# Performance work log

Hardware: AMD Instinct MI355X
Metric: run time of the kernel (lower is better)

## Reference

```python
import jax, jax.numpy as jnp
import numpy as np


def topk_activation(x, k):
    # x: [B, L]; keep top-k per row, zeros elsewhere (torch.topk + scatter_)
    vals, idx = jax.lax.top_k(x, k)            # [B, k]
    rows = jnp.arange(x.shape[0])[:, None]     # [B, 1]
    return jnp.zeros_like(x).at[rows, idx].set(vals)


def setup_inputs() -> dict:
    key = jax.random.key(0)
    k0, k1, k2, k3 = jax.random.split(key, 4)
    B, n_in, n_lat = 4096, 768, 24576
    x = jax.random.normal(k0, (B, n_in), dtype=jnp.float32)
    b = jnp.zeros((n_in,), jnp.float32)
    W_enc = jax.random.normal(k1, (n_lat, n_in), dtype=jnp.float32) * 0.02
    b_enc = jnp.zeros((n_lat,), jnp.float32)
    W_dec = jax.random.normal(k2, (n_in, n_lat), dtype=jnp.float32) * 0.02
    # unit L2 norm per decoder column (as in _normalize_decoder)
    W_dec = W_dec / jnp.clip(jnp.linalg.norm(W_dec, axis=0, keepdims=True), 1e-8)
    miss_counts = jax.random.randint(k3, (n_lat,), 0, 2)  # ~half 'dead' (>=1)
    return {"x": x, "b": b, "W_enc": W_enc, "b_enc": b_enc, "W_dec": W_dec,
            "miss_counts": miss_counts, "k": 32, "aux_k": 512}


def reference(x, b, W_enc, b_enc, W_dec, miss_counts, k, aux_k):
    x_centered = x - b                                   # [B, n_in]
    alpha_pre = x_centered @ W_enc.T + b_enc             # [B, n_lat]
    alpha = topk_activation(alpha_pre, k)                # sparse code
    x_hat = alpha @ W_dec.T + b                          # dense decode
    fired_mask = alpha != 0
    # aux dead-feature path; dead_mask = miss_counts >= threshold(=1).
    # With the chosen miss_counts fill, dead count >> aux_k, so
    # min(aux_k, dead.sum()) == aux_k (static for jit).
    dead_mask = miss_counts >= 1                         # [n_lat]
    alpha_pre_dead = jnp.where(dead_mask[None, :], alpha_pre, -jnp.inf)
    alpha_aux = topk_activation(alpha_pre_dead, aux_k)
    aux_x_hat = alpha_aux @ W_dec.T + b
    return x_hat, alpha, fired_mask, aux_x_hat
```

## Files before the change

kernel.cpp:

```cpp
#include <hip/hip_runtime.h>
#include <math.h>

#define NB   4096
#define NIN  768
#define NLAT 24576
#define K2   768
#define KT2  12

#define BM 128
#define BN 128
#define BK 16
#define LDT 132

#define CAND_CAP 512
#define BAND_CAP 160
#define MAIN_CAP 64
#define AUX_CAP  1024
#define SELT     1024
#define GRP      6

#define CM_CAP 768
#define CA_CAP 1536
#define BB_CAP 256
#define BPSTRIDE (BAND_CAP + 4)

#define OFF_K16  0
#define OFF_REDF 49152
#define OFF_CTRL 49664
#define OFF_PCNT 49792
#define OFF_CKM  50176
#define OFF_CIM  52224
#define OFF_CKA  54272
#define OFF_CIA  56320
#define OFF_BIM  58368
#define OFF_BIA  59008
#define OFF_BVM  59648
#define OFF_BVA  60928
#define OFF_BSM  62208
#define OFF_BSA  62368
#define OFF_REDI 62528
#define SMEM_SEL 62592

typedef __bf16 bf16x8 __attribute__((ext_vector_type(8)));
typedef float  f32x4  __attribute__((ext_vector_type(4)));

__device__ __forceinline__ unsigned fkey(float f) {
  unsigned u = __float_as_uint(f);
  return u ^ ((unsigned)((int)u >> 31) | 0x80000000u);
}
__device__ __forceinline__ float keyinv(unsigned u) {
  unsigned s = (u & 0x80000000u) ? (u ^ 0x80000000u) : ~u;
  return __uint_as_float(s);
}
__device__ __forceinline__ float zup(float p) {
  p = fminf(fmaxf(p, 1e-7f), 0.5f);
  float t = sqrtf(-2.0f * logf(p));
  return t - (2.30753f + 0.27061f * t) / (1.0f + 0.99229f * t + 0.04481f * t * t);
}

#define GLOAD16(g, l) __builtin_amdgcn_global_load_lds( \
    (const __attribute__((address_space(1))) unsigned int*)(g), \
    (__attribute__((address_space(3))) unsigned int*)(l), 16, 0, 0)

__global__ __launch_bounds__(256) void k_deadbits(const int* __restrict__ miss,
                                                  unsigned* __restrict__ bits) {
  int j = blockIdx.x * 256 + threadIdx.x;
  unsigned long long b = __ballot(miss[j] >= 1);
  if ((threadIdx.x & 63) == 0) {
    int w = j >> 5;
    bits[w] = (unsigned)b;
    bits[w + 1] = (unsigned)(b >> 32);
  }
}

__global__ __launch_bounds__(256) void k_ndead(const unsigned* __restrict__ bits,
                                               int* __restrict__ out) {
  __shared__ int w[4];
  int t = threadIdx.x;
  int c = 0;
  for (int i = t; i < NLAT / 32; i += 256) c += __popc(bits[i]);
#pragma unroll
  for (int o = 32; o; o >>= 1) c += __shfl_xor(c, o);
  if ((t & 63) == 0) w[t >> 6] = c;
  __syncthreads();
  if (t == 0) out[0] = w[0] + w[1] + w[2] + w[3];
}

__global__ __launch_bounds__(256) void k_transpose(const float* __restrict__ src,
                                                   __bf16* __restrict__ dst) {
  __shared__ float tile[32][33];
  int bx = blockIdx.x * 32;
  int by = blockIdx.y * 32;
  int tx = threadIdx.x, ty = threadIdx.y;
  for (int i = ty; i < 32; i += 8)
    tile[i][tx] = src[(size_t)(by + i) * NLAT + bx + tx];
  __syncthreads();
  for (int i = ty; i < 32; i += 8)
    dst[(size_t)(bx + i) * NIN + by + tx] = (__bf16)tile[tx][i];
}

__global__ __launch_bounds__(256) void k_pack_a(const float* __restrict__ x,
    const float* __restrict__ bvec, __bf16* __restrict__ A2) {
  const int mt = blockIdx.x, kt = blockIdx.y, t = threadIdx.x;
  __bf16* out = A2 + (((size_t)mt * KT2 + kt) << 13);
#pragma unroll
  for (int i = 0; i < 32; ++i) {
    int idx = i * 256 + t;
    int r = idx >> 6, c2 = idx & 63;
    int kk = c2 ^ ((r & 7) << 3);
    int k = kt * 64 + kk;
    float v = x[(size_t)(mt * 128 + r) * NIN + k] - bvec[k];
    out[idx] = (__bf16)v;
  }
}

__global__ __launch_bounds__(256) void k_pack_b(const float* __restrict__ We,
    __bf16* __restrict__ B2) {
  const int nt = blockIdx.x, kt = blockIdx.y, t = threadIdx.x;
  __bf16* out = B2 + (((size_t)nt * KT2 + kt) << 13);
#pragma unroll
  for (int i = 0; i < 32; ++i) {
    int idx = i * 256 + t;
    int r = idx >> 6, c2 = idx & 63;
    int kk = c2 ^ ((r & 7) << 3);
    int k = kt * 64 + kk;
    float v = We[(size_t)(nt * 128 + r) * NIN + k];
    out[idx] = (__bf16)v;
  }
}

__global__ __launch_bounds__(256) void k_gemm_bf16(
    const __bf16* __restrict__ A2, const __bf16* __restrict__ B2,
    const float* __restrict__ be, float* __restrict__ apre) {
  __shared__ char sA[16384];
  __shared__ char sB[16384];
  const int t = threadIdx.x;
  const int lane = t & 63, wave = t >> 6;
  int flat = blockIdx.y * 32 + blockIdx.x;
  int nf = (flat & 7) * 768 + (flat >> 3);
  const int mt = nf & 31, nt = nf >> 5;
  const int wm = wave >> 1, wn = wave & 1;

  int aoff[4][2], boff[4][2];
#pragma unroll
  for (int f = 0; f < 4; ++f) {
    int ra = wm * 64 + f * 16 + (lane & 15);
    int rb = wn * 64 + f * 16 + (lane & 15);
#pragma unroll
    for (int kk = 0; kk < 2; ++kk) {
      int c = kk * 64 + (lane >> 4) * 16;
      aoff[f][kk] = ra * 128 + (c ^ ((ra & 7) << 4));
      boff[f][kk] = rb * 128 + (c ^ ((rb & 7) << 4));
    }
  }
  f32x4 acc[4][4] = {};
  const char* gA = (const char*)(A2 + (((size_t)mt * KT2) << 13));
  const char* gB = (const char*)(B2 + (((size_t)nt * KT2) << 13));
  for (int kt = 0; kt < KT2; ++kt) {
    const char* tA = gA + ((size_t)kt << 14);
    const char* tB = gB + ((size_t)kt << 14);
#pragma unroll
    for (int i = 0; i < 4; ++i) {
      int chunk = (i * 4 + wave) * 1024;
      GLOAD16(tA + chunk + lane * 16, sA + chunk);
      GLOAD16(tB + chunk + lane * 16, sB + chunk);
    }
    __syncthreads();
#pragma unroll
    for (int kk = 0; kk < 2; ++kk) {
      bf16x8 a[4], b[4];
#pragma unroll
      for (int f = 0; f < 4; ++f) {
        a[f] = *(const bf16x8*)(sA + aoff[f][kk]);
        b[f] = *(const bf16x8*)(sB + boff[f][kk]);
      }
#pragma unroll
      for (int mi = 0; mi < 4; ++mi)
#pragma unroll
        for (int ni = 0; ni < 4; ++ni)
          acc[mi][ni] = __builtin_amdgcn_mfma_f32_16x16x32_bf16(a[mi], b[ni], acc[mi][ni], 0, 0, 0);
    }
    __syncthreads();
  }
  const int m0 = mt * 128 + wm * 64, n0 = nt * 128 + wn * 64;
#pragma unroll
  for (int ni = 0; ni < 4; ++ni) {
    int n = n0 + ni * 16 + (lane & 15);
    float bb = be[n];
#pragma unroll
    for (int mi = 0; mi < 4; ++mi) {
      int mbase = m0 + mi * 16 + (lane >> 4) * 4;
#pragma unroll
      for (int q = 0; q < 4; ++q)
        apre[(size_t)(mbase + q) * NLAT + n] = acc[mi][ni][q] + bb;
    }
  }
}

__global__ __launch_bounds__(256) void k_encgemm_f32(
    const float* __restrict__ x, const float* __restrict__ bvec,
    const float* __restrict__ We, const float* __restrict__ be,
    float* __restrict__ apre) {
  __shared__ float As[BK][LDT];
  __shared__ float Bs[BK][LDT];
  const int t = threadIdx.x;
  const int m0 = blockIdx.x * BM;
  const int n0 = blockIdx.y * BN;
  const int lane = t & 63, wave = t >> 6;
  const int cn = ((wave & 1) * 8 + (lane & 7)) * 8;
  const int cm = ((wave >> 1) * 8 + (lane >> 3)) * 8;
  float acc[8][8] = {};
  const float* xb = x + (size_t)m0 * NIN;
  const float* wb = We + (size_t)n0 * NIN;
  for (int k0 = 0; k0 < NIN; k0 += BK) {
#pragma unroll
    for (int i = 0; i < 2; ++i) {
      int e = t + i * 256;
      int row = e >> 2, q = e & 3;
      float4 bv = *(const float4*)(bvec + k0 + q * 4);
      float4 av = *(const float4*)(xb + (size_t)row * NIN + k0 + q * 4);
      av.x -= bv.x; av.y -= bv.y; av.z -= bv.z; av.w -= bv.w;
      As[q * 4 + 0][row] = av.x; As[q * 4 + 1][row] = av.y;
      As[q * 4 + 2][row] = av.z; As[q * 4 + 3][row] = av.w;
      float4 wv = *(const float4*)(wb + (size_t)row * NIN + k0 + q * 4);
      Bs[q * 4 + 0][row] = wv.x; Bs[q * 4 + 1][row] = wv.y;
      Bs[q * 4 + 2][row] = wv.z; Bs[q * 4 + 3][row] = wv.w;
    }
    __syncthreads();
#pragma unroll
    for (int kk = 0; kk < BK; ++kk) {
      float a0[8], b0[8];
      *(float4*)&a0[0] = *(const float4*)&As[kk][cm];
      *(float4*)&a0[4] = *(const float4*)&As[kk][cm + 4];
      *(float4*)&b0[0] = *(const float4*)&Bs[kk][cn];
      *(float4*)&b0[4] = *(const float4*)&Bs[kk][cn + 4];
#pragma unroll
      for (int i = 0; i < 8; ++i)
#pragma unroll
        for (int j = 0; j < 8; ++j)
          acc[i][j] = fmaf(a0[i], b0[j], acc[i][j]);
    }
    __syncthreads();
  }
  float bb[8];
  *(float4*)&bb[0] = *(const float4*)(be + n0 + cn);
  *(float4*)&bb[4] = *(const float4*)(be + n0 + cn + 4);
#pragma unroll
  for (int i = 0; i < 8; ++i) {
    float4 v0 = make_float4(acc[i][0] + bb[0], acc[i][1] + bb[1],
                            acc[i][2] + bb[2], acc[i][3] + bb[3]);
    float4 v1 = make_float4(acc[i][4] + bb[4], acc[i][5] + bb[5],
                            acc[i][6] + bb[6], acc[i][7] + bb[7]);
    float* orow = apre + (size_t)(m0 + cm + i) * NLAT + n0 + cn;
    *(float4*)orow = v0;
    *(float4*)(orow + 4) = v1;
  }
}

__global__ __launch_bounds__(1024) void k_select16(
    const float* __restrict__ apre, const float* __restrict__ x,
    const float* __restrict__ bvec, const float* __restrict__ We,
    const float* __restrict__ be, const unsigned* __restrict__ dbits,
    const int* __restrict__ kptr, const int* __restrict__ akptr,
    const int* __restrict__ ndeadP,
    int* __restrict__ cnts, int* __restrict__ mIdxG, float* __restrict__ mValG,
    int* __restrict__ aIdxG, float* __restrict__ aValG,
    int* __restrict__ bandP, int* __restrict__ flags) {
  __shared__ float redF[32];
  __shared__ float statF[4];
  __shared__ int ctrl[24];
  __shared__ int histM[256];
  __shared__ int histA[256];
  __shared__ uint2 cM[CM_CAP];
  __shared__ uint2 cA[CA_CAP];
  __shared__ uint2 bbM[BB_CAP];
  __shared__ uint2 bbA[BB_CAP];
  __shared__ int biM[BAND_CAP];
  __shared__ int biA[BAND_CAP];
  __shared__ double bvM[BAND_CAP];
  __shared__ double bvA[BAND_CAP];
  __shared__ unsigned char bsM[BAND_CAP];
  __shared__ unsigned char bsA[BAND_CAP];
  unsigned* uctrl = (unsigned*)ctrl;

  const int t = threadIdx.x;
  const int r = blockIdx.x;
  const int lane = t & 63, wave = t >> 6;

  if (t < 24) ctrl[t] = 0;
  if (t >= 256 && t < 512) histM[t - 256] = 0;
  else if (t >= 512 && t < 768) histA[t - 512] = 0;

  const uint4* rowp = (const uint4*)(apre + (size_t)r * NLAT);
  unsigned dm = 0;
  float s1 = 0.f, s2 = 0.f;
#pragma unroll
  for (int i = 0; i < GRP; ++i) {
    int g = t + SELT * i;
    uint4 rv = rowp[g];
    unsigned nb = (dbits[g >> 3] >> ((g & 7) * 4)) & 0xFu;
    dm |= nb << (4 * i);
    float vs[4] = {__uint_as_float(rv.x), __uint_as_float(rv.y),
                   __uint_as_float(rv.z), __uint_as_float(rv.w)};
#pragma unroll
    for (int q = 0; q < 4; ++q) { float v = vs[q]; s1 += v; s2 += v * v; }
  }
#pragma unroll
  for (int o = 32; o; o >>= 1) { s1 += __shfl_xor(s1, o); s2 += __shfl_xor(s2, o); }
  if (lane == 0) { redF[wave] = s1; redF[16 + wave] = s2; }
  __syncthreads();
  if (wave == 0) {
    float a0 = (lane < 16) ? redF[lane] : 0.f;
    float a1 = (lane < 16) ? redF[16 + lane] : 0.f;
#pragma unroll
    for (int o = 32; o; o >>= 1) { a0 += __shfl_xor(a0, o); a1 += __shfl_xor(a1, o); }
    if (lane == 0) {
      float mu = a0 / (float)NLAT;
      float var = fmaxf(a1 / (float)NLAT - mu * mu, 1e-20f);
      statF[0] = mu; statF[1] = sqrtf(var);
    }
  }
  __syncthreads();

  int kmain = kptr[0]; if (kmain > MAIN_CAP) kmain = MAIN_CAP;
  int kaux  = akptr[0]; if (kaux > AUX_CAP)  kaux  = AUX_CAP;
  const int ndead = ndeadP[0];
  int kauxE = kaux > ndead ? ndead : kaux;
  const bool mainOn = (kmain > 0);
  const bool auxOn  = (kauxE > 0);
  const float mu = statF[0], sg = statF[1];
  unsigned TkM = 0xFFFFFFFFu, TkA = 0xFFFFFFFFu;
  if (mainOn) TkM = fkey(mu + sg * zup(8.f * kmain / (float)NLAT));
  if (auxOn) {
    float facA = (3.f * kauxE > 1280.f) ? 2.f : 3.f;
    TkA = fkey(mu + sg * zup(facA * kauxE / (float)ndead));
  }

  unsigned mxM = 0u, mxA = 0u;
#pragma unroll
  for (int i = 0; i < GRP; ++i) {
    int g = t + SELT * i;
    uint4 rv = rowp[g];
    unsigned nb = (dm >> (4 * i)) & 0xFu;
    float vs[4] = {__uint_as_float(rv.x), __uint_as_float(rv.y),
                   __uint_as_float(rv.z), __uint_as_float(rv.w)};
#pragma unroll
    for (int q = 0; q < 4; ++q) {
      unsigned kk = fkey(vs[q]);
      unsigned j = (unsigned)(4 * g + q);
      if (mainOn && kk >= TkM) {
        mxM = kk > mxM ? kk : mxM;
        int p = atomicAdd(&ctrl[0], 1);
        if (p < CM_CAP) { cM[p].x = kk; cM[p].y = j; }
      }
      if (auxOn && ((nb >> q) & 1u) && kk >= TkA) {
        mxA = kk > mxA ? kk : mxA;
        int p = atomicAdd(&ctrl[1], 1);
        if (p < CA_CAP) { cA[p].x = kk; cA[p].y = j; }
      }
    }
  }
#pragma unroll
  for (int o = 32; o; o >>= 1) {
    unsigned a = __shfl_xor(mxM, o); mxM = a > mxM ? a : mxM;
    unsigned b = __shfl_xor(mxA, o); mxA = b > mxA ? b : mxA;
  }
  if (lane == 0) { atomicMax(&uctrl[10], mxM); atomicMax(&uctrl[11], mxA); }
  __syncthreads();
  int ccM = ctrl[0], ccA = ctrl[1];
  bool ok = (!mainOn || (ccM >= kmain && ccM <= CM_CAP)) &&
            (!auxOn  || (ccA >= kauxE && ccA <= CA_CAP));
  if (!ok) { if (t == 0) flags[r] = 1; return; }
  if (!auxOn) ccA = 0;
  if (!mainOn) ccM = 0;
  unsigned MxM = uctrl[10], MxA = uctrl[11];
  float sclM = 255.0f / fmaxf((float)(MxM - TkM) + 1.0f, 1.0f);
  float sclA = 255.0f / fmaxf((float)(MxA - TkA) + 1.0f, 1.0f);

  for (int c = t; c < ccM; c += 1024) {
    int b = (int)((float)(cM[c].x - TkM) * sclM);
    b = b < 0 ? 0 : (b > 255 ? 255 : b);
    atomicAdd(&histM[b], 1);
  }
  for (int c = t; c < ccA; c += 1024) {
    int b = (int)((float)(cA[c].x - TkA) * sclA);
    b = b < 0 ? 0 : (b > 255 ? 255 : b);
    atomicAdd(&histA[b], 1);
  }
  __syncthreads();
  if (t == 0 && mainOn) {
    int above = 0, b = 0;
    for (int i = 255; i >= 0; --i) {
      if (above + histM[i] >= kmain) { b = i; break; }
      above += histM[i];
    }
    ctrl[12] = b; ctrl[13] = above;
  }
  if (t == 64 && auxOn) {
    int above = 0, b = 0;
    for (int i = 255; i >= 0; --i) {
      if (above + histA[i] >= kauxE) { b = i; break; }
      above += histA[i];
    }
    ctrl[14] = b; ctrl[15] = above;
  }
  __syncthreads();
  int bM = ctrl[12], aboveM = ctrl[13];
  int bA = ctrl[14], aboveA = ctrl[15];
  for (int c = t; c < ccM; c += 1024) {
    int b = (int)((float)(cM[c].x - TkM) * sclM);
    b = b < 0 ? 0 : (b > 255 ? 255 : b);
    if (b == bM) {
      int p = atomicAdd(&ctrl[16], 1);
      if (p < BB_CAP) bbM[p] = cM[c];
    }
  }
  for (int c = t; c < ccA; c += 1024) {
    int b = (int)((float)(cA[c].x - TkA) * sclA);
    b = b < 0 ? 0 : (b > 255 ? 255 : b);
    if (b == bA) {
      int p = atomicAdd(&ctrl[17], 1);
      if (p < BB_CAP) bbA[p] = cA[c];
    }
  }
  __syncthreads();
  int nbM = ctrl[16], nbA = ctrl[17];
  if ((mainOn && nbM > BB_CAP) || (auxOn && nbA > BB_CAP)) {
    if (t == 0) flags[r] = 1;
    return;
  }
  if (!mainOn) nbM = 0;
  if (!auxOn) nbA = 0;
  if (t < nbM) {
    uint2 e = bbM[t];
    int rank = 0;
    for (int qq = 0; qq < nbM; ++qq) {
      uint2 f = bbM[qq];
      rank += (f.x > e.x || (f.x == e.x && (int)f.y < (int)e.y)) ? 1 : 0;
    }
    if (rank == kmain - aboveM - 1) ctrl[2] = (int)e.x;
  }
  if (t >= 512 && t - 512 < nbA) {
    uint2 e = bbA[t - 512];
    int rank = 0;
    for (int qq = 0; qq < nbA; ++qq) {
      uint2 f = bbA[qq];
      rank += (f.x > e.x || (f.x == e.x && (int)f.y < (int)e.y)) ? 1 : 0;
    }
    if (rank == kauxE - aboveA - 1) ctrl[3] = (int)e.x;
  }
  __syncthreads();

  float VsM = keyinv((unsigned)ctrl[2]);
  float epsM = 1.5e-2f + 2e-3f * fabsf(VsM);
  unsigned KhiBM = mainOn ? fkey(VsM + epsM) : 0xFFFFFFFFu;
  unsigned KloBM = mainOn ? fkey(VsM - epsM) : 0xFFFFFFFFu;
  float VsA = keyinv((unsigned)ctrl[3]);
  float epsA = 1.5e-2f + 2e-3f * fabsf(VsA);
  unsigned KhiBA = auxOn ? fkey(VsA + epsA) : 0xFFFFFFFFu;
  unsigned KloBA = auxOn ? fkey(VsA - epsA) : 0xFFFFFFFFu;
  for (int c = t; c < ccM; c += 1024) {
    unsigned kk = cM[c].x;
    if (kk > KhiBM) atomicAdd(&ctrl[4], 1);
    else if (kk >= KloBM) {
      int p = atomicAdd(&ctrl[5], 1);
      if (p < BAND_CAP) biM[p] = (int)cM[c].y;
    }
  }
  for (int c = t; c < ccA; c += 1024) {
    unsigned kk = cA[c].x;
    if (kk > KhiBA) atomicAdd(&ctrl[6], 1);
    else if (kk >= KloBA) {
      int p = atomicAdd(&ctrl[7], 1);
      if (p < BAND_CAP) biA[p] = (int)cA[c].y;
    }
  }
  __syncthreads();
  if ((mainOn && ctrl[5] > BAND_CAP) || (auxOn && ctrl[7] > BAND_CAP)) {
    if (t == 0) flags[r] = 1;
    return;
  }
  if (t == 0) flags[r] = 0;
  int nAbM = ctrl[4], bcM = ctrl[5];
  int nAbA = ctrl[6], bcA = ctrl[7];
  if (!mainOn) bcM = 0;
  if (!auxOn) bcA = 0;
  int needBM = kmain - nAbM; if (needBM < 0) needBM = 0; if (needBM > bcM) needBM = bcM;
  int needBA = kauxE - nAbA; if (needBA < 0) needBA = 0; if (needBA > bcA) needBA = bcA;

  {
    const float* xr = x + (size_t)r * NIN;
    float xb[NIN / 64];
#pragma unroll
    for (int jj = 0; jj < NIN / 64; ++jj) {
      int col = lane + 64 * jj;
      xb[jj] = xr[col] - bvec[col];
    }
    int tot = bcM + bcA;
    for (int m = wave; m < tot; m += 16) {
      int j = (m < bcM) ? biM[m] : biA[m - bcM];
      const float* wr = We + (size_t)j * NIN;
      double s = 0.0;
#pragma unroll
      for (int jj = 0; jj < NIN / 64; ++jj)
        s += (double)xb[jj] * (double)wr[lane + 64 * jj];
#pragma unroll
      for (int o = 32; o; o >>= 1) s += __shfl_xor(s, o);
      if (lane == 0) {
        if (m < bcM) bvM[m] = s + (double)be[j];
        else bvA[m - bcM] = s + (double)be[j];
      }
    }
  }
  __syncthreads();
  if (t < bcM) {
    double vi = bvM[t]; int ii = biM[t];
    double tie = fabs(vi) * 4e-8 + 1e-12;
    int rank = 0;
    for (int qq = 0; qq < bcM; ++qq) {
      double d = bvM[qq] - vi;
      rank += ((fabs(d) <= tie) ? (biM[qq] < ii) : (d > 0.0)) ? 1 : 0;
    }
    bsM[t] = (rank < needBM) ? 1 : 0;
  }
  if (t >= 512 && t - 512 < bcA) {
    int tt = t - 512;
    double vi = bvA[tt]; int ii = biA[tt];
    double tie = fabs(vi) * 4e-8 + 1e-12;
    int rank = 0;
    for (int qq = 0; qq < bcA; ++qq) {
      double d = bvA[qq] - vi;
      rank += ((fabs(d) <= tie) ? (biA[qq] < ii) : (d > 0.0)) ? 1 : 0;
    }
    bsA[tt] = (rank < needBA) ? 1 : 0;
  }
  __syncthreads();

  for (int c = t; c < ccM; c += 1024) {
    unsigned kk = cM[c].x; int j = (int)cM[c].y;
    bool sel = kk > KhiBM;
    if (!sel && kk >= KloBM) {
      for (int m2 = 0; m2 < bcM; ++m2)
        if (biM[m2] == j) { sel = bsM[m2] != 0; break; }
    }
    float v = keyinv(kk);
    if (sel && v != 0.0f) {
      int p = atomicAdd(&ctrl[8], 1);
      if (p < MAIN_CAP) { mIdxG[r * MAIN_CAP + p] = j; mValG[r * MAIN_CAP + p] = v; }
    }
  }
  for (int c = t; c < ccA; c += 1024) {
    unsigned kk = cA[c].x; int j = (int)cA[c].y;
    bool sel = kk > KhiBA;
    if (!sel && kk >= KloBA) {
      for (int m2 = 0; m2 < bcA; ++m2)
        if (biA[m2] == j) { sel = bsA[m2] != 0; break; }
    }
    float v = keyinv(kk);
    if (sel && v != 0.0f) {
      int p = atomicAdd(&ctrl[9], 1);
      if (p < AUX_CAP) { aIdxG[r * AUX_CAP + p] = j; aValG[r * AUX_CAP + p] = v; }
    }
  }
  __syncthreads();
  int* bp = bandP + (size_t)r * BPSTRIDE;
  if (t == 0) {
    cnts[2 * r] = ctrl[8] < MAIN_CAP ? ctrl[8] : MAIN_CAP;
    cnts[2 * r + 1] = auxOn ? (ctrl[9] < AUX_CAP ? ctrl[9] : AUX_CAP) : 0;
    bp[0] = (int)KhiBM; bp[1] = (int)KloBM; bp[2] = bcM;
  }
  if (t < bcM) bp[3 + t] = (biM[t] << 1) | (int)bsM[t];
}

__global__ __launch_bounds__(256) void k_emit(
    const float* apre, const int* __restrict__ flags,
    const int* __restrict__ bandP, float* __restrict__ alpha, float* mask) {
  const int bid = blockIdx.x;
  const int r = bid / 3, c = bid % 3;
  if (flags[r]) return;
  __shared__ int hdr[3];
  __shared__ int bent[BAND_CAP];
  const int t = threadIdx.x;
  const int* bp = bandP + (size_t)r * BPSTRIDE;
  if (t < 3) hdr[t] = bp[t];
  __syncthreads();
  int bc = hdr[2];
  if (t < bc) bent[t] = bp[3 + t];
  __syncthreads();
  unsigned KhiB = (unsigned)hdr[0], KloB = (unsigned)hdr[1];
  const float4* src = (const float4*)(apre + (size_t)r * NLAT) + c * 2048;
  float4* adst = (float4*)(alpha + (size_t)r * NLAT) + c * 2048;
  float4* mdst = (float4*)(mask + (size_t)r * NLAT) + c * 2048;
  const int ebase = c * 8192;
#pragma unroll
  for (int i = 0; i < 8; ++i) {
    int g = t + 256 * i;
    float4 v4 = src[g];
    float vs[4] = {v4.x, v4.y, v4.z, v4.w};
    float av[4], mv[4];
#pragma unroll
    for (int q = 0; q < 4; ++q) {
      float v = vs[q];
      unsigned kk = fkey(v);
      int j = ebase + 4 * g + q;
      bool sel = kk > KhiB;
      if (!sel && kk >= KloB) {
        for (int m = 0; m < bc; ++m)
          if ((bent[m] >> 1) == j) { sel = (bent[m] & 1) != 0; break; }
      }
      av[q] = sel ? v : 0.0f;
      mv[q] = (sel && v != 0.0f) ? 1.0f : 0.0f;
    }
    adst[g] = make_float4(av[0], av[1], av[2], av[3]);
    mdst[g] = make_float4(mv[0], mv[1], mv[2], mv[3]);
  }
}

__global__ __launch_bounds__(SELT) void k_selectFB(
    const float* apre, const float* __restrict__ x,
    const float* __restrict__ bvec, const float* __restrict__ We,
    const float* __restrict__ be, const unsigned* __restrict__ dbits,
    const int* __restrict__ kptr, const int* __restrict__ akptr,
    float* __restrict__ alpha, float* mask,
    int* __restrict__ cnts, int* __restrict__ mIdxG, float* __restrict__ mValG,
    int* __restrict__ aIdxG, float* __restrict__ aValG,
    const int* __restrict__ flags) {
  if (flags[blockIdx.x] == 0) return;
  extern __shared__ char smem[];
  uint2*    keys2 = (uint2*)(smem + OFF_K16);
  float*    redF  = (float*)(smem + OFF_REDF);
  int*      redI  = (int*)(smem + OFF_REDI);
  int*      ctrl  = (int*)(smem + OFF_CTRL);
  float*    ctrlF = (float*)(smem + OFF_CTRL);
  int*      pcnt  = (int*)(smem + OFF_PCNT);
  unsigned* ckM   = (unsigned*)(smem + OFF_CKM);
  int*      ciM   = (int*)(smem + OFF_CIM);
  unsigned* ckA   = (unsigned*)(smem + OFF_CKA);
  int*      ciA   = (int*)(smem + OFF_CIA);
  int*      biM   = (int*)(smem + OFF_BIM);
  int*      biA   = (int*)(smem + OFF_BIA);
  double*   bvM   = (double*)(smem + OFF_BVM);
  double*   bvA   = (double*)(smem + OFF_BVA);
  unsigned char* bsM = (unsigned char*)(smem + OFF_BSM);
  unsigned char* bsA = (unsigned char*)(smem + OFF_BSA);

  const int t = threadIdx.x;
  const int r = blockIdx.x;
  const int lane = t & 63, wave = t >> 6;

  if (t < 96) pcnt[t] = 0;
  else if (t < 108) ctrl[t - 96] = 0;

  const uint4* rowp = (const uint4*)(apre + (size_t)r * NLAT);
  const float* rowf = apre + (size_t)r * NLAT;
  unsigned dm = 0;
  float s1 = 0.f, s2 = 0.f;
  float vmxA = -INFINITY, vmnA = INFINITY, vmxD = -INFINITY, vmnD = INFINITY;
#pragma unroll
  for (int i = 0; i < GRP; ++i) {
    int g = t + SELT * i;
    uint4 rv = rowp[g];
    unsigned nb = (dbits[g >> 3] >> ((g & 7) * 4)) & 0xFu;
    dm |= nb << (4 * i);
    float vs[4] = {__uint_as_float(rv.x), __uint_as_float(rv.y),
                   __uint_as_float(rv.z), __uint_as_float(rv.w)};
    unsigned k16[4];
#pragma unroll
    for (int q = 0; q < 4; ++q) {
      float v = vs[q];
      k16[q] = fkey(v) >> 16;
      s1 += v; s2 += v * v;
      vmxA = fmaxf(vmxA, v); vmnA = fminf(vmnA, v);
      if ((nb >> q) & 1u) { vmxD = fmaxf(vmxD, v); vmnD = fminf(vmnD, v); }
    }
    uint2 kp2;
    kp2.x = k16[0] | (k16[1] << 16);
    kp2.y = k16[2] | (k16[3] << 16);
    keys2[g] = kp2;
  }
  int nd = __popc(dm & 0xFFFFFFu);
#pragma unroll
  for (int o = 32; o; o >>= 1) {
    s1 += __shfl_xor(s1, o); s2 += __shfl_xor(s2, o);
    vmxA = fmaxf(vmxA, __shfl_xor(vmxA, o)); vmnA = fminf(vmnA, __shfl_xor(vmnA, o));
    vmxD = fmaxf(vmxD, __shfl_xor(vmxD, o)); vmnD = fminf(vmnD, __shfl_xor(vmnD, o));
    nd += __shfl_xor(nd, o);
  }
  if (lane == 0) {
    float* rf = redF + wave * 8;
    rf[0] = s1; rf[1] = s2; rf[2] = vmxA; rf[3] = vmnA; rf[4] = vmxD; rf[5] = vmnD;
    redI[wave] = nd;
  }
  __syncthreads();
  if (wave == 0) {
    float a0 = 0.f, a1 = 0.f, a2 = -INFINITY, a3 = INFINITY, a4 = -INFINITY, a5 = INFINITY;
    int a6 = 0;
    if (lane < 16) {
      const float* rf = redF + lane * 8;
      a0 = rf[0]; a1 = rf[1]; a2 = rf[2]; a3 = rf[3]; a4 = rf[4]; a5 = rf[5];
      a6 = redI[lane];
    }
#pragma unroll
    for (int o = 32; o; o >>= 1) {
      a0 += __shfl_xor(a0, o); a1 += __shfl_xor(a1, o);
      a2 = fmaxf(a2, __shfl_xor(a2, o)); a3 = fminf(a3, __shfl_xor(a3, o));
      a4 = fmaxf(a4, __shfl_xor(a4, o)); a5 = fminf(a5, __shfl_xor(a5, o));
      a6 += __shfl_xor(a6, o);
    }
    if (lane == 0) {
      float mu = a0 / (float)NLAT;
      float var = fmaxf(a1 / (float)NLAT - mu * mu, 1e-20f);
      ctrlF[16] = mu; ctrlF[17] = sqrtf(var);
      ctrlF[18] = a3; ctrlF[19] = a2;
      ctrlF[20] = a5; ctrlF[21] = a4;
      ctrl[22] = a6;
    }
  }
  __syncthreads();

  int kmain = kptr[0]; if (kmain > MAIN_CAP) kmain = MAIN_CAP;
  int kaux  = akptr[0]; if (kaux > AUX_CAP)  kaux  = AUX_CAP;
  const float mu = ctrlF[16], sg = ctrlF[17];
  const int ndead = ctrl[22];
  int kauxE = kaux > ndead ? ndead : kaux;
  const bool mainOn = (kmain > 0);
  const bool auxOn  = (kauxE > 0);

  unsigned TloM = fkey(ctrlF[18]) >> 16, ThiM = (fkey(ctrlF[19]) >> 16) + 1u;
  int cLoM = NLAT, cHiM = 0;
  unsigned TloA = 0u, ThiA = 2u;
  int cLoA = 0, cHiA = 0;
  if (auxOn) { TloA = fkey(ctrlF[20]) >> 16; ThiA = (fkey(ctrlF[21]) >> 16) + 1u; cLoA = ndead; }

  for (int it = 0; it < 16; ++it) {
    bool actM = mainOn && (cLoM - cHiM) > (CAND_CAP - 8) && (ThiM - TloM) > 1u;
    bool actA = auxOn  && (cLoA - cHiA) > (CAND_CAP - 8) && (ThiA - TloA) > 1u;
    if (!actM && !actA) break;
    unsigned TM1 = TloM + 1u, TM2 = TM1, TM3 = TM1;
    unsigned TA1 = TloA + 1u, TA2 = TA1, TA3 = TA1;
    if (actM) {
      unsigned lo1 = TloM + 1u, hi1 = ThiM - 1u;
      if (it == 0) {
        float fn = (float)NLAT;
        TM1 = fkey(mu + sg * zup(4.f * kmain / fn)) >> 16;
        TM2 = fkey(mu + sg * zup((float)kmain / fn)) >> 16;
        TM3 = fkey(mu + sg * zup(0.25f * kmain / fn)) >> 16;
      } else {
        float vlo = keyinv(TloM << 16), vhi = keyinv((ThiM << 16) - 1u);
        TM1 = fkey(0.75f * vlo + 0.25f * vhi) >> 16;
        TM2 = fkey(0.50f * vlo + 0.50f * vhi) >> 16;
        TM3 = fkey(0.25f * vlo + 0.75f * vhi) >> 16;
      }
      TM1 = TM1 < lo1 ? lo1 : (TM1 > hi1 ? hi1 : TM1);
      TM2 = TM2 < TM1 ? TM1 : (TM2 > hi1 ? hi1 : TM2);
      TM3 = TM3 < TM2 ? TM2 : (TM3 > hi1 ? hi1 : TM3);
    }
    if (actA) {
      unsigned lo1 = TloA + 1u, hi1 = ThiA - 1u;
      if (it == 0) {
        float fn = (float)ndead;
        TA1 = fkey(mu + sg * zup(4.f * kauxE / fn)) >> 16;
        TA2 = fkey(mu + sg * zup((float)kauxE / fn)) >> 16;
        TA3 = fkey(mu + sg * zup(0.25f * kauxE / fn)) >> 16;
      } else {
        float vlo = keyinv(TloA << 16), vhi = keyinv((ThiA << 16) - 1u);
        TA1 = fkey(0.75f * vlo + 0.25f * vhi) >> 16;
        TA2 = fkey(0.50f * vlo + 0.50f * vhi) >> 16;
        TA3 = fkey(0.25f * vlo + 0.75f * vhi) >> 16;
      }
      TA1 = TA1 < lo1 ? lo1 : (TA1 > hi1 ? hi1 : TA1);
      TA2 = TA2 < TA1 ? TA1 : (TA2 > hi1 ? hi1 : TA2);
      TA3 = TA3 < TA2 ? TA2 : (TA3 > hi1 ? hi1 : TA3);
    }
    int cm1 = 0, cm2 = 0, cm3 = 0, ca1 = 0, ca2 = 0, ca3 = 0;
#pragma unroll
    for (int i = 0; i < GRP; ++i) {
      uint2 kv = keys2[t + SELT * i];
      unsigned nb = (dm >> (4 * i)) & 0xFu;
      unsigned ks[4] = {kv.x & 0xFFFFu, kv.x >> 16, kv.y & 0xFFFFu, kv.y >> 16};
#pragma unroll
      for (int q = 0; q < 4; ++q) {
        unsigned kk = ks[q];
        cm1 += (kk >= TM1); cm2 += (kk >= TM2); cm3 += (kk >= TM3);
        if ((nb >> q) & 1u) { ca1 += (kk >= TA1); ca2 += (kk >= TA2); ca3 += (kk >= TA3); }
      }
    }
#pragma unroll
    for (int o = 32; o; o >>= 1) {
      cm1 += __shfl_xor(cm1, o); cm2 += __shfl_xor(cm2, o); cm3 += __shfl_xor(cm3, o);
      ca1 += __shfl_xor(ca1, o); ca2 += __shfl_xor(ca2, o); ca3 += __shfl_xor(ca3, o);
    }
    if (lane == 0) {
      int* pc = pcnt + it * 6;
      atomicAdd(&pc[0], cm1); atomicAdd(&pc[1], cm2); atomicAdd(&pc[2], cm3);
      atomicAdd(&pc[3], ca1); atomicAdd(&pc[4], ca2); atomicAdd(&pc[5], ca3);
    }
    __syncthreads();
    const int* pc = pcnt + it * 6;
    int CM1 = pc[0], CM2 = pc[1], CM3 = pc[2];
    int CA1 = pc[3], CA2 = pc[4], CA3 = pc[5];
    if (actM) {
      if (CM3 >= kmain)      { TloM = TM3; cLoM = CM3; }
      else if (CM2 >= kmain) { TloM = TM2; cLoM = CM2; ThiM = TM3; cHiM = CM3; }
      else if (CM1 >= kmain) { TloM = TM1; cLoM = CM1; ThiM = TM2; cHiM = CM2; }
      else                   { ThiM = TM1; cHiM = CM1; }
    }
    if (actA) {
      if (CA3 >= kauxE)      { TloA = TA3; cLoA = CA3; }
      else if (CA2 >= kauxE) { TloA = TA2; cLoA = CA2; ThiA = TA3; cHiA = CA3; }
      else if (CA1 >= kauxE) { TloA = TA1; cLoA = CA1; ThiA = TA2; cHiA = CA2; }
      else                   { ThiA = TA1; cHiA = CA1; }
    }
  }

#pragma unroll
  for (int i = 0; i < GRP; ++i) {
    int g = t + SELT * i;
    uint2 kv = keys2[g];
    unsigned nb = (dm >> (4 * i)) & 0xFu;
    unsigned ks[4] = {kv.x & 0xFFFFu, kv.x >> 16, kv.y & 0xFFFFu, kv.y >> 16};
#pragma unroll
    for (int q = 0; q < 4; ++q) {
      unsigned kk = ks[q];
      int j = 4 * g + q;
      if (mainOn && kk >= TloM && kk < ThiM) {
        int p = atomicAdd(&ctrl[0], 1);
        if (p < CAND_CAP) { ckM[p] = fkey(rowf[j]); ciM[p] = j; }
      }
      if (auxOn && ((nb >> q) & 1u) && kk >= TloA && kk < ThiA) {
        int p = atomicAdd(&ctrl[1], 1);
        if (p < CAND_CAP) { ckA[p] = fkey(rowf[j]); ciA[p] = j; }
      }
    }
  }
  __syncthreads();
  int ccM = ctrl[0] < CAND_CAP ? ctrl[0] : CAND_CAP;
  int ccA = ctrl[1] < CAND_CAP ? ctrl[1] : CAND_CAP;
  int needM = kmain - cHiM; if (needM < 1) needM = 1; if (needM > ccM) needM = ccM;
  int needA = kauxE - cHiA; if (needA < 1) needA = 1; if (needA > ccA) needA = ccA;

  if (t < ccM) {
    unsigned ki = ckM[t]; int ii = ciM[t];
    int rank = 0;
    for (int qq = 0; qq < ccM; ++qq) {
      unsigned kq = ckM[qq];
      rank += (kq > ki || (kq == ki && ciM[qq] < ii)) ? 1 : 0;
    }
    if (rank == needM - 1) ctrl[2] = (int)ki;
  } else if (t >= 512 && t - 512 < ccA) {
    int tt = t - 512;
    unsigned ki = ckA[tt]; int ii = ciA[tt];
    int rank = 0;
    for (int qq = 0; qq < ccA; ++qq) {
      unsigned kq = ckA[qq];
      rank += (kq > ki || (kq == ki && ciA[qq] < ii)) ? 1 : 0;
    }
    if (rank == needA - 1) ctrl[3] = (int)ki;
  }
  __syncthreads();

  float VsM = keyinv((unsigned)ctrl[2]);
  float epsM = 1.5e-2f + 2e-3f * fabsf(VsM);
  unsigned KhiBM = mainOn ? fkey(VsM + epsM) : 0xFFFFFFFFu;
  unsigned KloBM = mainOn ? fkey(VsM - epsM) : 0xFFFFFFFFu;
  float VsA = keyinv((unsigned)ctrl[3]);
  float epsA = 1.5e-2f + 2e-3f * fabsf(VsA);
  unsigned KhiBA = auxOn ? fkey(VsA + epsA) : 0xFFFFFFFFu;
  unsigned KloBA = auxOn ? fkey(VsA - epsA) : 0xFFFFFFFFu;
  unsigned KhiBM16 = KhiBM >> 16, KloBM16 = KloBM >> 16;
  unsigned KhiBA16 = KhiBA >> 16, KloBA16 = KloBA >> 16;
  int abvM = 0, abvA = 0;
#pragma unroll
  for (int i = 0; i < GRP; ++i) {
    int g = t + SELT * i;
    uint2 kv = keys2[g];
    unsigned nb = (dm >> (4 * i)) & 0xFu;
    unsigned ks[4] = {kv.x & 0xFFFFu, kv.x >> 16, kv.y & 0xFFFFu, kv.y >> 16};
#pragma unroll
    for (int q = 0; q < 4; ++q) {
      unsigned kk = ks[q];
      int j = 4 * g + q;
      if (mainOn) {
        if (kk > KhiBM16) ++abvM;
        else if (kk >= KloBM16) {
          unsigned kf = fkey(rowf[j]);
          if (kf > KhiBM) ++abvM;
          else if (kf >= KloBM) {
            int p = atomicAdd(&ctrl[5], 1);
            if (p < BAND_CAP) biM[p] = j;
          }
        }
      }
      if (auxOn && ((nb >> q) & 1u)) {
        if (kk > KhiBA16) ++abvA;
        else if (kk >= KloBA16) {
          unsigned kf = fkey(rowf[j]);
          if (kf > KhiBA) ++abvA;
          else if (kf >= KloBA) {
            int p = atomicAdd(&ctrl[7], 1);
            if (p < BAND_CAP) biA[p] = j;
          }
        }
      }
    }
  }
#pragma unroll
  for (int o = 32; o; o >>= 1) { abvM += __shfl_xor(abvM, o); abvA += __shfl_xor(abvA, o); }
  if (lane == 0) { atomicAdd(&ctrl[4], abvM); atomicAdd(&ctrl[6], abvA); }
  __syncthreads();
  int nAbM = ctrl[4], bcM = ctrl[5] < BAND_CAP ? ctrl[5] : BAND_CAP;
  int nAbA = ctrl[6], bcA = auxOn ? (ctrl[7] < BAND_CAP ? ctrl[7] : BAND_CAP) : 0;
  if (!mainOn) bcM = 0;
  int needBM = kmain - nAbM; if (needBM < 0) needBM = 0; if (needBM > bcM) needBM = bcM;
  int needBA = kauxE - nAbA; if (needBA < 0) needBA = 0; if (needBA > bcA) needBA = bcA;

  {
    const float* xr = x + (size_t)r * NIN;
    float xb[NIN / 64];
#pragma unroll
    for (int jj = 0; jj < NIN / 64; ++jj) {
      int col = lane + 64 * jj;
      xb[jj] = xr[col] - bvec[col];
    }
    int tot = bcM + bcA;
    for (int m = wave; m < tot; m += 16) {
      int j = (m < bcM) ? biM[m] : biA[m - bcM];
      const float* wr = We + (size_t)j * NIN;
      double s = 0.0;
#pragma unroll
      for (int jj = 0; jj < NIN / 64; ++jj)
        s += (double)xb[jj] * (double)wr[lane + 64 * jj];
#pragma unroll
      for (int o = 32; o; o >>= 1) s += __shfl_xor(s, o);
      if (lane == 0) {
        if (m < bcM) bvM[m] = s + (double)be[j];
        else bvA[m - bcM] = s + (double)be[j];
      }
    }
  }
  __syncthreads();
  if (t < bcM) {
    double vi = bvM[t]; int ii = biM[t];
    double tie = fabs(vi) * 4e-8 + 1e-12;
    int rank = 0;
    for (int qq = 0; qq < bcM; ++qq) {
      double d = bvM[qq] - vi;
      rank += ((fabs(d) <= tie) ? (biM[qq] < ii) : (d > 0.0)) ? 1 : 0;
    }
    bsM[t] = (rank < needBM) ? 1 : 0;
  } else if (t >= 512 && t - 512 < bcA) {
    int tt = t - 512;
    double vi = bvA[tt]; int ii = biA[tt];
    double tie = fabs(vi) * 4e-8 + 1e-12;
    int rank = 0;
    for (int qq = 0; qq < bcA; ++qq) {
      double d = bvA[qq] - vi;
      rank += ((fabs(d) <= tie) ? (biA[qq] < ii) : (d > 0.0)) ? 1 : 0;
    }
    bsA[tt] = (rank < needBA) ? 1 : 0;
  }
  __syncthreads();

  {
    float4* arow = (float4*)(alpha + (size_t)r * NLAT);
    float4* mrow = (float4*)(mask + (size_t)r * NLAT);
#pragma unroll
    for (int i = 0; i < GRP; ++i) {
      int g = t + SELT * i;
      uint4 rv = rowp[g];
      unsigned nb = (dm >> (4 * i)) & 0xFu;
      float vs[4] = {__uint_as_float(rv.x), __uint_as_float(rv.y),
                     __uint_as_float(rv.z), __uint_as_float(rv.w)};
      float av[4], mv[4];
#pragma unroll
      for (int q = 0; q < 4; ++q) {
        float v = vs[q];
        unsigned kk = fkey(v);
        int j = 4 * g + q;
        bool selM = mainOn && (kk > KhiBM);
        if (mainOn && !selM && kk >= KloBM) {
          for (int m2 = 0; m2 < bcM; ++m2)
            if (biM[m2] == j) { selM = bsM[m2] != 0; break; }
        }
        bool nz = selM && (v != 0.0f);
        av[q] = selM ? v : 0.0f;
        mv[q] = nz ? 1.0f : 0.0f;
        if (nz) {
          int p = atomicAdd(&ctrl[8], 1);
          if (p < MAIN_CAP) { mIdxG[r * MAIN_CAP + p] = j; mValG[r * MAIN_CAP + p] = v; }
        }
        if (auxOn && ((nb >> q) & 1u)) {
          bool selA = kk > KhiBA;
          if (!selA && kk >= KloBA) {
            for (int m2 = 0; m2 < bcA; ++m2)
              if (biA[m2] == j) { selA = bsA[m2] != 0; break; }
          }
          if (selA && v != 0.0f) {
            int p = atomicAdd(&ctrl[9], 1);
            if (p < AUX_CAP) { aIdxG[r * AUX_CAP + p] = j; aValG[r * AUX_CAP + p] = v; }
          }
        }
      }
      arow[g] = make_float4(av[0], av[1], av[2], av[3]);
      mrow[g] = make_float4(mv[0], mv[1], mv[2], mv[3]);
    }
  }
  __syncthreads();
  if (t == 0) {
    cnts[2 * r] = ctrl[8] < MAIN_CAP ? ctrl[8] : MAIN_CAP;
    cnts[2 * r + 1] = auxOn ? (ctrl[9] < AUX_CAP ? ctrl[9] : AUX_CAP) : 0;
  }
}

__global__ __launch_bounds__(256) void k_decode(
    const int* __restrict__ cnts, const int* __restrict__ mIdxG,
    const float* __restrict__ mValG, const int* __restrict__ aIdxG,
    const float* __restrict__ aValG, const float* __restrict__ bvec,
    const __bf16* __restrict__ Wt, const float* __restrict__ Wd,
    float* __restrict__ xhat, float* __restrict__ auxo) {
  const int r = blockIdx.x, t = threadIdx.x;
  __shared__ int sMi[MAIN_CAP];
  __shared__ float sMv[MAIN_CAP];
  __shared__ int sAi[AUX_CAP];
  __shared__ float sAv[AUX_CAP];
  int kc = cnts[2 * r], ac = cnts[2 * r + 1];
  if (t < MAIN_CAP && t < kc) { sMi[t] = mIdxG[r * MAIN_CAP + t]; sMv[t] = mValG[r * MAIN_CAP + t]; }
  for (int i = t; i < ac; i += 256) { sAi[i] = aIdxG[r * AUX_CAP + i]; sAv[i] = aValG[r * AUX_CAP + i]; }
  __syncthreads();

  float o0 = 0.f, o1 = 0.f, o2 = 0.f;
  float a0 = 0.f, a1 = 0.f, a2 = 0.f;
  if (Wt) {
    int i = 0;
    for (; i + 4 <= kc; i += 4) {
      int i0 = sMi[i], i1 = sMi[i + 1], i2 = sMi[i + 2], i3 = sMi[i + 3];
      float v0 = sMv[i], v1 = sMv[i + 1], v2 = sMv[i + 2], v3 = sMv[i + 3];
      const __bf16* p0 = Wt + (size_t)i0 * NIN;
      const __bf16* p1 = Wt + (size_t)i1 * NIN;
      const __bf16* p2 = Wt + (size_t)i2 * NIN;
      const __bf16* p3 = Wt + (size_t)i3 * NIN;
      float w00 = p0[t], w01 = p0[t + 256], w02 = p0[t + 512];
      float w10 = p1[t], w11 = p1[t + 256], w12 = p1[t + 512];
      float w20 = p2[t], w21 = p2[t + 256], w22 = p2[t + 512];
      float w30 = p3[t], w31 = p3[t + 256], w32 = p3[t + 512];
      o0 = fmaf(v0, w00, o0); o1 = fmaf(v0, w01, o1); o2 = fmaf(v0, w02, o2);
      o0 = fmaf(v1, w10, o0); o1 = fmaf(v1, w11, o1); o2 = fmaf(v1, w12, o2);
      o0 = fmaf(v2, w20, o0); o1 = fmaf(v2, w21, o1); o2 = fmaf(v2, w22, o2);
      o0 = fmaf(v3, w30, o0); o1 = fmaf(v3, w31, o1); o2 = fmaf(v3, w32, o2);
    }
    for (; i < kc; ++i) {
      const __bf16* p = Wt + (size_t)sMi[i] * NIN;
      float v = sMv[i];
      o0 = fmaf(v, (float)p[t], o0);
      o1 = fmaf(v, (float)p[t + 256], o1);
      o2 = fmaf(v, (float)p[t + 512], o2);
    }
    i = 0;
    for (; i + 4 <= ac; i += 4) {
      int i0 = sAi[i], i1 = sAi[i + 1], i2 = sAi[i + 2], i3 = sAi[i + 3];
      float v0 = sAv[i], v1 = sAv[i + 1], v2 = sAv[i + 2], v3 = sAv[i + 3];
      const __bf16* p0 = Wt + (size_t)i0 * NIN;
      const __bf16* p1 = Wt + (size_t)i1 * NIN;
      const __bf16* p2 = Wt + (size_t)i2 * NIN;
      const __bf16* p3 = Wt + (size_t)i3 * NIN;
      float w00 = p0[t], w01 = p0[t + 256], w02 = p0[t + 512];
      float w10 = p1[t], w11 = p1[t + 256], w12 = p1[t + 512];
      float w20 = p2[t], w21 = p2[t + 256], w22 = p2[t + 512];
      float w30 = p3[t], w31 = p3[t + 256], w32 = p3[t + 512];
      a0 = fmaf(v0, w00, a0); a1 = fmaf(v0, w01, a1); a2 = fmaf(v0, w02, a2);
      a0 = fmaf(v1, w10, a0); a1 = fmaf(v1, w11, a1); a2 = fmaf(v1, w12, a2);
      a0 = fmaf(v2, w20, a0); a1 = fmaf(v2, w21, a1); a2 = fmaf(v2, w22, a2);
      a0 = fmaf(v3, w30, a0); a1 = fmaf(v3, w31, a1); a2 = fmaf(v3, w32, a2);
    }
    for (; i < ac; ++i) {
      const __bf16* p = Wt + (size_t)sAi[i] * NIN;
      float v = sAv[i];
      a0 = fmaf(v, (float)p[t], a0);
      a1 = fmaf(v, (float)p[t + 256], a1);
      a2 = fmaf(v, (float)p[t + 512], a2);
    }
  } else {
    for (int i = 0; i < kc; ++i) {
      float v = sMv[i]; int ix = sMi[i];
      o0 = fmaf(v, Wd[(size_t)t * NLAT + ix], o0);
      o1 = fmaf(v, Wd[(size_t)(t + 256) * NLAT + ix], o1);
      o2 = fmaf(v, Wd[(size_t)(t + 512) * NLAT + ix], o2);
    }
    for (int i = 0; i < ac; ++i) {
      float v = sAv[i]; int ix = sAi[i];
      a0 = fmaf(v, Wd[(size_t)t * NLAT + ix], a0);
      a1 = fmaf(v, Wd[(size_t)(t + 256) * NLAT + ix], a1);
      a2 = fmaf(v, Wd[(size_t)(t + 512) * NLAT + ix], a2);
    }
  }
  float b0 = bvec[t], b1 = bvec[t + 256], b2 = bvec[t + 512];
  xhat[(size_t)r * NIN + t] = o0 + b0;
  xhat[(size_t)r * NIN + t + 256] = o1 + b1;
  xhat[(size_t)r * NIN + t + 512] = o2 + b2;
  auxo[(size_t)r * NIN + t] = a0 + b0;
  auxo[(size_t)r * NIN + t + 256] = a1 + b1;
  auxo[(size_t)r * NIN + t + 512] = a2 + b2;
}

extern "C" void kernel_launch(void* const* d_in, const int* in_sizes, int n_in,
                              void* d_out, int out_size, void* d_ws, size_t ws_size,
                              hipStream_t stream) {
  const float* x  = (const float*)d_in[0];
  const float* bv = (const float*)d_in[1];
  const float* We = (const float*)d_in[2];
  const float* be = (const float*)d_in[3];
  const float* Wd = (const float*)d_in[4];
  const int* miss = (const int*)d_in[5];
  const int* kp   = (const int*)d_in[6];
  const int* akp  = (const int*)d_in[7];

  float* out   = (float*)d_out;
  float* xhat  = out;
  float* alpha = out + (size_t)3145728;
  float* apre  = out + (size_t)103809024;
  float* auxo  = out + (size_t)204472320;

  char* wsb = (char*)d_ws;
  size_t o = 0;
  unsigned* dbits = (unsigned*)(wsb + o); o += 65536;
  int*   cnts  = (int*)(wsb + o); o += 65536;
  int*   mIdxG = (int*)(wsb + o); o += (size_t)NB * MAIN_CAP * 4;
  float* mValG = (float*)(wsb + o); o += (size_t)NB * MAIN_CAP * 4;
  int*   aIdxG = (int*)(wsb + o); o += (size_t)NB * AUX_CAP * 4;
  float* aValG = (float*)(wsb + o); o += (size_t)NB * AUX_CAP * 4;
  int*   bandP = (int*)(wsb + o); o += (size_t)NB * BPSTRIDE * 4;
  int*   flags = (int*)(wsb + o); o += 65536;
  int*   ndead = (int*)(wsb + o); o += 65536;
  size_t offWt = o;
  size_t offA2 = offWt + (size_t)NLAT * NIN * 2;
  size_t offB2 = offA2 + (size_t)NB * K2 * 2;
  size_t needFull = offB2 + (size_t)NLAT * K2 * 2;
  bool haveWt   = ws_size >= offA2;
  bool haveFull = ws_size >= needFull;
  __bf16* Wt = haveWt ? (__bf16*)(wsb + offWt) : nullptr;
  __bf16* A2 = (__bf16*)(wsb + offA2);
  __bf16* B2 = (__bf16*)(wsb + offB2);

  k_deadbits<<<96, 256, 0, stream>>>(miss, dbits);
  k_ndead<<<1, 256, 0, stream>>>(dbits, ndead);
  if (haveFull) {
    k_pack_a<<<dim3(32, KT2), 256, 0, stream>>>(x, bv, A2);
    k_pack_b<<<dim3(192, KT2), 256, 0, stream>>>(We, B2);
  }
  if (haveWt)
    k_transpose<<<dim3(NLAT / 32, NIN / 32), dim3(32, 8), 0, stream>>>(Wd, Wt);

  if (haveFull)
    k_gemm_bf16<<<dim3(32, 192), 256, 0, stream>>>(A2, B2, be, apre);
  else
    k_encgemm_f32<<<dim3(NB / BM, NLAT / BN), 256, 0, stream>>>(x, bv, We, be, apre);

  k_select16<<<NB, 1024, 0, stream>>>(apre, x, bv, We, be, dbits, kp, akp, ndead,
                                      cnts, mIdxG, mValG, aIdxG, aValG, bandP, flags);
  k_selectFB<<<NB, SELT, SMEM_SEL, stream>>>(apre, x, bv, We, be, dbits, kp, akp,
                                             alpha, apre, cnts, mIdxG, mValG,
                                             aIdxG, aValG, flags);
  k_emit<<<NB * 3, 256, 0, stream>>>(apre, flags, bandP, alpha, apre);
  k_decode<<<NB, 256, 0, stream>>>(cnts, mIdxG, mValG, aIdxG, aValG, bv,
                                   Wt, Wd, xhat, auxo);
}
```

Baseline: 1.400 ms.

## Fuse per-row mean/variance statistics into the encoder GEMM epilogue

The per-row sum and sum-of-squares of alpha_pre are now computed in the bf16 GEMM epilogue. Each wave reduces its partials with shuffles and adds them into a global rowStats buffer with float atomics. The selection kernel then reads these statistics instead of making its own full pass over each 96KB row, removing one read of the large activation matrix. The costs are extra epilogue work, atomics, and order-dependent rounding in the stats that feed the selection thresholds; the fp32 fallback path gets a separate stats kernel.

```diff
diff --git a/kernel.cpp b/kernel.cpp
--- a/kernel.cpp
+++ b/kernel.cpp
@@ -63,7 +63,8 @@
     (__attribute__((address_space(3))) unsigned int*)(l), 16, 0, 0)
 
 __global__ __launch_bounds__(256) void k_deadbits(const int* __restrict__ miss,
-                                                  unsigned* __restrict__ bits) {
+                                                  unsigned* __restrict__ bits,
+                                                  float* __restrict__ rowStats) {
   int j = blockIdx.x * 256 + threadIdx.x;
   unsigned long long b = __ballot(miss[j] >= 1);
   if ((threadIdx.x & 63) == 0) {
@@ -71,6 +72,7 @@
     bits[w] = (unsigned)b;
     bits[w + 1] = (unsigned)(b >> 32);
   }
+  if (j < 2 * NB) rowStats[j] = 0.0f;
 }
 
 __global__ __launch_bounds__(256) void k_ndead(const unsigned* __restrict__ bits,
@@ -84,6 +86,27 @@
   if ((t & 63) == 0) w[t >> 6] = c;
   __syncthreads();
   if (t == 0) out[0] = w[0] + w[1] + w[2] + w[3];
+}
+
+__global__ __launch_bounds__(256) void k_rowstats(const float* __restrict__ apre,
+                                                  float* __restrict__ rowStats) {
+  const int r = blockIdx.x, t = threadIdx.x;
+  const float4* rowp = (const float4*)(apre + (size_t)r * NLAT);
+  float s1 = 0.f, s2 = 0.f;
+  for (int g = t; g < NLAT / 4; g += 256) {
+    float4 v = rowp[g];
+    s1 += v.x + v.y + v.z + v.w;
+    s2 += v.x * v.x + v.y * v.y + v.z * v.z + v.w * v.w;
+  }
+#pragma unroll
+  for (int o = 32; o; o >>= 1) { s1 += __shfl_xor(s1, o); s2 += __shfl_xor(s2, o); }
+  __shared__ float w1[4], w2[4];
+  if ((t & 63) == 0) { w1[t >> 6] = s1; w2[t >> 6] = s2; }
+  __syncthreads();
+  if (t == 0) {
+    rowStats[2 * r] = w1[0] + w1[1] + w1[2] + w1[3];
+    rowStats[2 * r + 1] = w2[0] + w2[1] + w2[2] + w2[3];
+  }
 }
 
 __global__ __launch_bounds__(256) void k_transpose(const float* __restrict__ src,
@@ -131,7 +154,8 @@
 
 __global__ __launch_bounds__(256) void k_gemm_bf16(
     const __bf16* __restrict__ A2, const __bf16* __restrict__ B2,
-    const float* __restrict__ be, float* __restrict__ apre) {
+    const float* __restrict__ be, float* __restrict__ apre,
+    float* __restrict__ rowStats) {
   __shared__ char sA[16384];
   __shared__ char sB[16384];
   const int t = threadIdx.x;
@@ -183,6 +207,7 @@
     __syncthreads();
   }
   const int m0 = mt * 128 + wm * 64, n0 = nt * 128 + wn * 64;
+  float ps1[16] = {}, ps2[16] = {};
 #pragma unroll
   for (int ni = 0; ni < 4; ++ni) {
     int n = n0 + ni * 16 + (lane & 15);
@@ -191,8 +216,28 @@
     for (int mi = 0; mi < 4; ++mi) {
       int mbase = m0 + mi * 16 + (lane >> 4) * 4;
 #pragma unroll
-      for (int q = 0; q < 4; ++q)
-        apre[(size_t)(mbase + q) * NLAT + n] = acc[mi][ni][q] + bb;
+      for (int q = 0; q < 4; ++q) {
+        float v = acc[mi][ni][q] + bb;
+        apre[(size_t)(mbase + q) * NLAT + n] = v;
+        ps1[mi * 4 + q] += v;
+        ps2[mi * 4 + q] += v * v;
+      }
+    }
+  }
+#pragma unroll
+  for (int i = 0; i < 16; ++i) {
+#pragma unroll
+    for (int o = 1; o < 16; o <<= 1) {
+      ps1[i] += __shfl_xor(ps1[i], o);
+      ps2[i] += __shfl_xor(ps2[i], o);
+    }
+  }
+  if ((lane & 15) == 0) {
+#pragma unroll
+    for (int i = 0; i < 16; ++i) {
+      int row = m0 + (i >> 2) * 16 + (lane >> 4) * 4 + (i & 3);
+      atomicAdd(&rowStats[2 * row], ps1[i]);
+      atomicAdd(&rowStats[2 * row + 1], ps2[i]);
     }
   }
 }
@@ -257,17 +302,15 @@
   }
 }
 
-__global__ __launch_bounds__(1024) void k_select16(
+__global__ __launch_bounds__(1024) void k_select17(
     const float* __restrict__ apre, const float* __restrict__ x,
     const float* __restrict__ bvec, const float* __restrict__ We,
     const float* __restrict__ be, const unsigned* __restrict__ dbits,
     const int* __restrict__ kptr, const int* __restrict__ akptr,
-    const int* __restrict__ ndeadP,
+    const int* __restrict__ ndeadP, const float* __restrict__ rowStats,
     int* __restrict__ cnts, int* __restrict__ mIdxG, float* __restrict__ mValG,
     int* __restrict__ aIdxG, float* __restrict__ aValG,
     int* __restrict__ bandP, int* __restrict__ flags) {
-  __shared__ float redF[32];
-  __shared__ float statF[4];
   __shared__ int ctrl[24];
   __shared__ int histM[256];
   __shared__ int histA[256];
@@ -290,36 +333,6 @@
   if (t < 24) ctrl[t] = 0;
   if (t >= 256 && t < 512) histM[t - 256] = 0;
   else if (t >= 512 && t < 768) histA[t - 512] = 0;
-
-  const uint4* rowp = (const uint4*)(apre + (size_t)r * NLAT);
-  unsigned dm = 0;
-  float s1 = 0.f, s2 = 0.f;
-#pragma unroll
-  for (int i = 0; i < GRP; ++i) {
-    int g = t + SELT * i;
-    uint4 rv = rowp[g];
-    unsigned nb = (dbits[g >> 3] >> ((g & 7) * 4)) & 0xFu;
-    dm |= nb << (4 * i);
-    float vs[4] = {__uint_as_float(rv.x), __uint_as_float(rv.y),
-                   __uint_as_float(rv.z), __uint_as_float(rv.w)};
-#pragma unroll
-    for (int q = 0; q < 4; ++q) { float v = vs[q]; s1 += v; s2 += v * v; }
-  }
-#pragma unroll
-  for (int o = 32; o; o >>= 1) { s1 += __shfl_xor(s1, o); s2 += __shfl_xor(s2, o); }
-  if (lane == 0) { redF[wave] = s1; redF[16 + wave] = s2; }
-  __syncthreads();
-  if (wave == 0) {
-    float a0 = (lane < 16) ? redF[lane] : 0.f;
-    float a1 = (lane < 16) ? redF[16 + lane] : 0.f;
-#pragma unroll
-    for (int o = 32; o; o >>= 1) { a0 += __shfl_xor(a0, o); a1 += __shfl_xor(a1, o); }
-    if (lane == 0) {
-      float mu = a0 / (float)NLAT;
-      float var = fmaxf(a1 / (float)NLAT - mu * mu, 1e-20f);
-      statF[0] = mu; statF[1] = sqrtf(var);
-    }
-  }
   __syncthreads();
 
   int kmain = kptr[0]; if (kmain > MAIN_CAP) kmain = MAIN_CAP;
@@ -328,7 +341,9 @@
   int kauxE = kaux > ndead ? ndead : kaux;
   const bool mainOn = (kmain > 0);
   const bool auxOn  = (kauxE > 0);
-  const float mu = statF[0], sg = statF[1];
+  const float s1 = rowStats[2 * r], s2 = rowStats[2 * r + 1];
+  const float mu = s1 / (float)NLAT;
+  const float sg = sqrtf(fmaxf(s2 / (float)NLAT - mu * mu, 1e-20f));
   unsigned TkM = 0xFFFFFFFFu, TkA = 0xFFFFFFFFu;
   if (mainOn) TkM = fkey(mu + sg * zup(8.f * kmain / (float)NLAT));
   if (auxOn) {
@@ -336,12 +351,13 @@
     TkA = fkey(mu + sg * zup(facA * kauxE / (float)ndead));
   }
 
+  const uint4* rowp = (const uint4*)(apre + (size_t)r * NLAT);
   unsigned mxM = 0u, mxA = 0u;
 #pragma unroll
   for (int i = 0; i < GRP; ++i) {
     int g = t + SELT * i;
     uint4 rv = rowp[g];
-    unsigned nb = (dm >> (4 * i)) & 0xFu;
+    unsigned nb = (dbits[g >> 3] >> ((g & 7) * 4)) & 0xFu;
     float vs[4] = {__uint_as_float(rv.x), __uint_as_float(rv.y),
                    __uint_as_float(rv.z), __uint_as_float(rv.w)};
 #pragma unroll
@@ -1131,6 +1147,7 @@
   int*   bandP = (int*)(wsb + o); o += (size_t)NB * BPSTRIDE * 4;
   int*   flags = (int*)(wsb + o); o += 65536;
   int*   ndead = (int*)(wsb + o); o += 65536;
+  float* rowStats = (float*)(wsb + o); o += (size_t)NB * 2 * 4;
   size_t offWt = o;
   size_t offA2 = offWt + (size_t)NLAT * NIN * 2;
   size_t offB2 = offA2 + (size_t)NB * K2 * 2;
@@ -1141,7 +1158,7 @@
   __bf16* A2 = (__bf16*)(wsb + offA2);
   __bf16* B2 = (__bf16*)(wsb + offB2);
 
-  k_deadbits<<<96, 256, 0, stream>>>(miss, dbits);
+  k_deadbits<<<96, 256, 0, stream>>>(miss, dbits, rowStats);
   k_ndead<<<1, 256, 0, stream>>>(dbits, ndead);
   if (haveFull) {
     k_pack_a<<<dim3(32, KT2), 256, 0, stream>>>(x, bv, A2);
@@ -1150,13 +1167,16 @@
   if (haveWt)
     k_transpose<<<dim3(NLAT / 32, NIN / 32), dim3(32, 8), 0, stream>>>(Wd, Wt);
 
-  if (haveFull)
-    k_gemm_bf16<<<dim3(32, 192), 256, 0, stream>>>(A2, B2, be, apre);
-  else
+  if (haveFull) {
+    k_gemm_bf16<<<dim3(32, 192), 256, 0, stream>>>(A2, B2, be, apre, rowStats);
+  } else {
     k_encgemm_f32<<<dim3(NB / BM, NLAT / BN), 256, 0, stream>>>(x, bv, We, be, apre);
-
-  k_select16<<<NB, 1024, 0, stream>>>(apre, x, bv, We, be, dbits, kp, akp, ndead,
-                                      cnts, mIdxG, mValG, aIdxG, aValG, bandP, flags);
+    k_rowstats<<<NB, 256, 0, stream>>>(apre, rowStats);
+  }
+
+  k_select17<<<NB, 1024, 0, stream>>>(apre, x, bv, We, be, dbits, kp, akp, ndead,
+                                      rowStats, cnts, mIdxG, mValG, aIdxG, aValG,
+                                      bandP, flags);
   k_selectFB<<<NB, SELT, SMEM_SEL, stream>>>(apre, x, bv, We, be, dbits, kp, akp,
                                              alpha, apre, cnts, mIdxG, mValG,
                                              aIdxG, aValG, flags);
```

Measured after the change: 1.463 ms. 4.5% more time.
